# Kernel optimization log

Hardware: AMD Instinct MI355X
Metric: run time of the kernel (lower is better)

The kernel has to match this reference:

```python
import jax, jax.numpy as jnp
import numpy as np
import math

NUM_HEADS = 32
NUM_KV_HEADS = 8
HEAD_DIM = 128
Q_MULT = NUM_HEADS // NUM_KV_HEADS  # 4
CACHE_LEN = 4096
BATCH = 16


def setup_inputs() -> dict:
    key = jax.random.key(0)
    ks = jax.random.split(key, 5)
    return {
        "Q": jax.random.normal(ks[0], (BATCH, 1, NUM_HEADS * HEAD_DIM), dtype=jnp.float32),
        "K": jax.random.normal(ks[1], (BATCH, 1, NUM_KV_HEADS * HEAD_DIM), dtype=jnp.float32),
        "V": jax.random.normal(ks[2], (BATCH, 1, NUM_KV_HEADS * HEAD_DIM), dtype=jnp.float32),
        "K_cache": jax.random.normal(ks[3], (BATCH, CACHE_LEN, NUM_KV_HEADS, HEAD_DIM), dtype=jnp.float32),
        "V_cache": jax.random.normal(ks[4], (BATCH, CACHE_LEN, NUM_KV_HEADS, HEAD_DIM), dtype=jnp.float32),
        "attention_mask": jnp.zeros((BATCH, 1, 1, CACHE_LEN), dtype=jnp.float32),
    }


def reference(Q, K, V, K_cache, V_cache, attention_mask):
    b = Q.shape[0]
    scale = 1.0 / math.sqrt(HEAD_DIM)
    # Q: (b, kv_heads, q_mult, head_dim) -- group query heads by kv head (GQA)
    Qh = Q.reshape(b, NUM_KV_HEADS, Q_MULT, HEAD_DIM) * scale
    # caches -> (b, kv_heads, S, d); append new token's K/V -> S+1
    Kc = jnp.transpose(K_cache, (0, 2, 1, 3))
    Vc = jnp.transpose(V_cache, (0, 2, 1, 3))
    Kn = jnp.transpose(K.reshape(b, 1, NUM_KV_HEADS, HEAD_DIM), (0, 2, 1, 3))
    Vn = jnp.transpose(V.reshape(b, 1, NUM_KV_HEADS, HEAD_DIM), (0, 2, 1, 3))
    K_full = jnp.concatenate([Kc, Kn], axis=2)  # (b, kv, S+1, d)
    V_full = jnp.concatenate([Vc, Vn], axis=2)
    # scores: (b, kv, q_mult, S+1) -- GQA broadcast instead of repeat_interleave
    scores = jnp.einsum("bkgd,bksd->bkgs", Qh, K_full)
    # additive mask padded with 0 for the newly appended position
    m = jnp.pad(attention_mask[:, 0, 0, :], ((0, 0), (0, 1)))  # (b, S+1)
    scores = scores + m[:, None, None, :]
    w = jax.nn.softmax(scores, axis=-1)
    out = jnp.einsum("bkgs,bksd->bkgd", w, V_full)  # (b, kv, q_mult, d)
    return out.reshape(b, 1, NUM_HEADS * HEAD_DIM)
```

## Files before the change

kernel.cpp:

```cpp
#include <hip/hip_runtime.h>
#include <math.h>

#define BATCH 16
#define KVH   8
#define QM    4
#define HD    128
#define SLEN  4096

__global__ __launch_bounds__(256, 4) void attn_partial(
    const float* __restrict__ Q, const float* __restrict__ Kn,
    const float* __restrict__ Vn, const float* __restrict__ Kc,
    const float* __restrict__ Vc, const float* __restrict__ Mask,
    float* __restrict__ Op, float* __restrict__ Lp,
    int nseg, int seglen)
{
    const int tid  = threadIdx.x;
    const int wave = tid >> 6;
    const int lane = tid & 63;
    const int g    = lane >> 4;
    const int c    = lane & 15;
    const int kv   = blockIdx.y;
    const int b    = blockIdx.z;
    const int seg  = blockIdx.x * 4 + wave;

    const float scale = 0.088388347648318447f;

    const float* qb = Q + (size_t)b * (KVH * QM * HD) + kv * (QM * HD) + c * 4;
    float4 q[QM][2];
#pragma unroll
    for (int h = 0; h < QM; ++h) {
#pragma unroll
        for (int j = 0; j < 2; ++j) {
            float4 t = *(const float4*)(qb + h * HD + j * 64);
            q[h][j].x = t.x * scale; q[h][j].y = t.y * scale;
            q[h][j].z = t.z * scale; q[h][j].w = t.w * scale;
        }
    }

    float  l[QM] = {0.f, 0.f, 0.f, 0.f};
    float4 o[QM][2];
#pragma unroll
    for (int h = 0; h < QM; ++h)
#pragma unroll
        for (int j = 0; j < 2; ++j) o[h][j] = make_float4(0.f, 0.f, 0.f, 0.f);

    const size_t rowstride = (size_t)KVH * HD;
    const float* kc   = Kc + (size_t)b * SLEN * rowstride + kv * HD + c * 4;
    const float* vc   = Vc + (size_t)b * SLEN * rowstride + kv * HD + c * 4;
    const float* mrow = Mask + (size_t)b * SLEN;

    const int start = seg * seglen;
    const int niter = seglen >> 2;

    for (int i = 0; i < niter; ++i) {
        const int pos = start + i * 4 + g;
        const float* kp = kc + (size_t)pos * rowstride;
        const float* vp = vc + (size_t)pos * rowstride;
        float4 k0 = *(const float4*)(kp);
        float4 k1 = *(const float4*)(kp + 64);
        float4 v0 = *(const float4*)(vp);
        float4 v1 = *(const float4*)(vp + 64);
        float  mk = mrow[pos];

        float s[QM];
#pragma unroll
        for (int h = 0; h < QM; ++h)
            s[h] = q[h][0].x * k0.x + q[h][0].y * k0.y + q[h][0].z * k0.z + q[h][0].w * k0.w
                 + q[h][1].x * k1.x + q[h][1].y * k1.y + q[h][1].z * k1.z + q[h][1].w * k1.w;

#pragma unroll
        for (int off = 1; off <= 8; off <<= 1) {
#pragma unroll
            for (int h = 0; h < QM; ++h) s[h] += __shfl_xor(s[h], off);
        }

#pragma unroll
        for (int h = 0; h < QM; ++h) {
            float w = __expf(s[h] + mk);
            l[h] += w;
            o[h][0].x += w * v0.x; o[h][0].y += w * v0.y;
            o[h][0].z += w * v0.z; o[h][0].w += w * v0.w;
            o[h][1].x += w * v1.x; o[h][1].y += w * v1.y;
            o[h][1].z += w * v1.z; o[h][1].w += w * v1.w;
        }
    }

    if (seg == nseg - 1) {
        const float* kp = Kn + (size_t)b * (KVH * HD) + kv * HD + c * 4;
        const float* vp = Vn + (size_t)b * (KVH * HD) + kv * HD + c * 4;
        float4 k0 = *(const float4*)(kp);
        float4 k1 = *(const float4*)(kp + 64);
        float4 v0 = *(const float4*)(vp);
        float4 v1 = *(const float4*)(vp + 64);
        float s[QM];
#pragma unroll
        for (int h = 0; h < QM; ++h)
            s[h] = q[h][0].x * k0.x + q[h][0].y * k0.y + q[h][0].z * k0.z + q[h][0].w * k0.w
                 + q[h][1].x * k1.x + q[h][1].y * k1.y + q[h][1].z * k1.z + q[h][1].w * k1.w;
#pragma unroll
        for (int off = 1; off <= 8; off <<= 1) {
#pragma unroll
            for (int h = 0; h < QM; ++h) s[h] += __shfl_xor(s[h], off);
        }
        const float gate = (g == 0) ? 1.f : 0.f;
#pragma unroll
        for (int h = 0; h < QM; ++h) {
            float w = __expf(s[h]) * gate;
            l[h] += w;
            o[h][0].x += w * v0.x; o[h][0].y += w * v0.y;
            o[h][0].z += w * v0.z; o[h][0].w += w * v0.w;
            o[h][1].x += w * v1.x; o[h][1].y += w * v1.y;
            o[h][1].z += w * v1.z; o[h][1].w += w * v1.w;
        }
    }

#pragma unroll
    for (int off = 16; off <= 32; off <<= 1) {
#pragma unroll
        for (int h = 0; h < QM; ++h) {
            l[h]      += __shfl_xor(l[h],      off);
            o[h][0].x += __shfl_xor(o[h][0].x, off);
            o[h][0].y += __shfl_xor(o[h][0].y, off);
            o[h][0].z += __shfl_xor(o[h][0].z, off);
            o[h][0].w += __shfl_xor(o[h][0].w, off);
            o[h][1].x += __shfl_xor(o[h][1].x, off);
            o[h][1].y += __shfl_xor(o[h][1].y, off);
            o[h][1].z += __shfl_xor(o[h][1].z, off);
            o[h][1].w += __shfl_xor(o[h][1].w, off);
        }
    }

    const size_t sidx = ((size_t)b * KVH + kv) * nseg + seg;
    if (g == 0) {
#pragma unroll
        for (int h = 0; h < QM; ++h) {
            float* op = Op + (sidx * QM + h) * HD + c * 4;
            *(float4*)(op)      = o[h][0];
            *(float4*)(op + 64) = o[h][1];
            if (c == 0) Lp[sidx * QM + h] = l[h];
        }
    }
}

__global__ __launch_bounds__(HD) void attn_combine(
    const float* __restrict__ Op, const float* __restrict__ Lp,
    float* __restrict__ out, int nseg)
{
    const int d  = threadIdx.x;
    const int h  = blockIdx.x & (QM - 1);
    const int kv = (blockIdx.x >> 2) & (KVH - 1);
    const int b  = blockIdx.x >> 5;
    const size_t base = ((size_t)b * KVH + kv) * nseg;

    float acc = 0.f, L = 0.f;
    for (int cseg = 0; cseg < nseg; ++cseg) {
        acc += Op[(base + cseg) * QM * HD + h * HD + d];
        L   += Lp[(base + cseg) * QM + h];
    }
    out[((size_t)b * KVH * QM + kv * QM + h) * HD + d] = acc / L;
}

extern "C" void kernel_launch(void* const* d_in, const int* in_sizes, int n_in,
                              void* d_out, int out_size, void* d_ws, size_t ws_size,
                              hipStream_t stream)
{
    const float* Q    = (const float*)d_in[0];
    const float* K    = (const float*)d_in[1];
    const float* V    = (const float*)d_in[2];
    const float* Kc   = (const float*)d_in[3];
    const float* Vc   = (const float*)d_in[4];
    const float* Mask = (const float*)d_in[5];
    float* out = (float*)d_out;

    int nseg = 64;
    const size_t per_seg = (size_t)BATCH * KVH * QM * (HD + 1) * sizeof(float);
    while (nseg > 4 && (size_t)nseg * per_seg > ws_size) nseg >>= 1;
    const int seglen = SLEN / nseg;

    float* Op = (float*)d_ws;
    float* Lp = Op + (size_t)nseg * BATCH * KVH * QM * HD;

    dim3 grid1(nseg / 4, KVH, BATCH);
    attn_partial<<<grid1, 256, 0, stream>>>(Q, K, V, Kc, Vc, Mask, Op, Lp, nseg, seglen);
    attn_combine<<<dim3(BATCH * KVH * QM), HD, 0, stream>>>(Op, Lp, out, nseg);
}
```

Measured before the change: 547.4 us.

## Software-pipeline K loads and process two positions per lane per iteration

The partial-attention loop now handles two cache positions per 16-lane group each iteration and prefetches the next iteration's K rows and mask values into registers while the current V rows are loaded and consumed. The aim is more memory-level parallelism per wave, hiding global-load latency on this bandwidth-bound decode attention. In exchange, register use rises, so launch bounds drop to 3 blocks per SM, which may lower occupancy. The last iteration issues a redundant prefetch of the segment start, and the minimum segment count is raised to 8 so each segment has at least 8 positions.

After: 545.2 us. No clear change (-0.4%).

```diff
diff --git a/kernel.cpp b/kernel.cpp
--- a/kernel.cpp
+++ b/kernel.cpp
@@ -7,7 +7,7 @@
 #define HD    128
 #define SLEN  4096
 
-__global__ __launch_bounds__(256, 4) void attn_partial(
+__global__ __launch_bounds__(256, 3) void attn_partial(
     const float* __restrict__ Q, const float* __restrict__ Kn,
     const float* __restrict__ Vn, const float* __restrict__ Kc,
     const float* __restrict__ Vc, const float* __restrict__ Mask,
@@ -50,39 +50,73 @@
     const float* mrow = Mask + (size_t)b * SLEN;
 
     const int start = seg * seglen;
-    const int niter = seglen >> 2;
+    const int niter = seglen >> 3;
+
+    int pA = start + g * 2;
+    const float* kpA = kc + (size_t)pA * rowstride;
+    const float* kpB = kpA + rowstride;
+    float4 ka0 = *(const float4*)(kpA);
+    float4 ka1 = *(const float4*)(kpA + 64);
+    float4 kb0 = *(const float4*)(kpB);
+    float4 kb1 = *(const float4*)(kpB + 64);
+    float  ma  = mrow[pA];
+    float  mb  = mrow[pA + 1];
 
     for (int i = 0; i < niter; ++i) {
-        const int pos = start + i * 4 + g;
-        const float* kp = kc + (size_t)pos * rowstride;
-        const float* vp = vc + (size_t)pos * rowstride;
-        float4 k0 = *(const float4*)(kp);
-        float4 k1 = *(const float4*)(kp + 64);
-        float4 v0 = *(const float4*)(vp);
-        float4 v1 = *(const float4*)(vp + 64);
-        float  mk = mrow[pos];
-
-        float s[QM];
-#pragma unroll
-        for (int h = 0; h < QM; ++h)
-            s[h] = q[h][0].x * k0.x + q[h][0].y * k0.y + q[h][0].z * k0.z + q[h][0].w * k0.w
-                 + q[h][1].x * k1.x + q[h][1].y * k1.y + q[h][1].z * k1.z + q[h][1].w * k1.w;
-
+        const int pos = start + i * 8 + g * 2;
+
+        const float* vpA = vc + (size_t)pos * rowstride;
+        const float* vpB = vpA + rowstride;
+        float4 va0 = *(const float4*)(vpA);
+        float4 va1 = *(const float4*)(vpA + 64);
+        float4 vb0 = *(const float4*)(vpB);
+        float4 vb1 = *(const float4*)(vpB + 64);
+
+        int pn = pos + 8;
+        if (i + 1 == niter) pn = start + g * 2;
+        const float* kpAn = kc + (size_t)pn * rowstride;
+        const float* kpBn = kpAn + rowstride;
+        float4 nka0 = *(const float4*)(kpAn);
+        float4 nka1 = *(const float4*)(kpAn + 64);
+        float4 nkb0 = *(const float4*)(kpBn);
+        float4 nkb1 = *(const float4*)(kpBn + 64);
+        float  nma  = mrow[pn];
+        float  nmb  = mrow[pn + 1];
+
+        float sA[QM], sB[QM];
+#pragma unroll
+        for (int h = 0; h < QM; ++h) {
+            sA[h] = q[h][0].x * ka0.x + q[h][0].y * ka0.y + q[h][0].z * ka0.z + q[h][0].w * ka0.w
+                  + q[h][1].x * ka1.x + q[h][1].y * ka1.y + q[h][1].z * ka1.z + q[h][1].w * ka1.w;
+            sB[h] = q[h][0].x * kb0.x + q[h][0].y * kb0.y + q[h][0].z * kb0.z + q[h][0].w * kb0.w
+                  + q[h][1].x * kb1.x + q[h][1].y * kb1.y + q[h][1].z * kb1.z + q[h][1].w * kb1.w;
+        }
 #pragma unroll
         for (int off = 1; off <= 8; off <<= 1) {
 #pragma unroll
-            for (int h = 0; h < QM; ++h) s[h] += __shfl_xor(s[h], off);
-        }
-
-#pragma unroll
-        for (int h = 0; h < QM; ++h) {
-            float w = __expf(s[h] + mk);
-            l[h] += w;
-            o[h][0].x += w * v0.x; o[h][0].y += w * v0.y;
-            o[h][0].z += w * v0.z; o[h][0].w += w * v0.w;
-            o[h][1].x += w * v1.x; o[h][1].y += w * v1.y;
-            o[h][1].z += w * v1.z; o[h][1].w += w * v1.w;
-        }
+            for (int h = 0; h < QM; ++h) {
+                sA[h] += __shfl_xor(sA[h], off);
+                sB[h] += __shfl_xor(sB[h], off);
+            }
+        }
+
+#pragma unroll
+        for (int h = 0; h < QM; ++h) {
+            float wA = __expf(sA[h] + ma);
+            float wB = __expf(sB[h] + mb);
+            l[h] += wA + wB;
+            o[h][0].x += wA * va0.x + wB * vb0.x;
+            o[h][0].y += wA * va0.y + wB * vb0.y;
+            o[h][0].z += wA * va0.z + wB * vb0.z;
+            o[h][0].w += wA * va0.w + wB * vb0.w;
+            o[h][1].x += wA * va1.x + wB * vb1.x;
+            o[h][1].y += wA * va1.y + wB * vb1.y;
+            o[h][1].z += wA * va1.z + wB * vb1.z;
+            o[h][1].w += wA * va1.w + wB * vb1.w;
+        }
+
+        ka0 = nka0; ka1 = nka1; kb0 = nkb0; kb1 = nkb1;
+        ma = nma; mb = nmb;
     }
 
     if (seg == nseg - 1) {
@@ -174,7 +208,7 @@
 
     int nseg = 64;
     const size_t per_seg = (size_t)BATCH * KVH * QM * (HD + 1) * sizeof(float);
-    while (nseg > 4 && (size_t)nseg * per_seg > ws_size) nseg >>= 1;
+    while (nseg > 8 && (size_t)nseg * per_seg > ws_size) nseg >>= 1;
     const int seglen = SLEN / nseg;
 
     float* Op = (float*)d_ws;
```
